# Optimization experiments

Measured on AMD Instinct MI355X. Metric: run time of the kernel, lower is better.

Reference implementation:

```python
import jax, jax.numpy as jnp
import numpy as np

INPUT, HIDDEN, OUTPUT = 128, 256, 128
BATCH, SEQ = 64, 2048


def setup_inputs() -> dict:
    key = jax.random.key(0)
    ks = jax.random.split(key, 7)
    s_ih = 1.0 / np.sqrt(HIDDEN)
    x = jax.random.normal(ks[0], (BATCH, SEQ, INPUT), dtype=jnp.float32)
    W_ih = jax.random.uniform(ks[1], (HIDDEN, INPUT), jnp.float32, -s_ih, s_ih)
    W_hh = jax.random.uniform(ks[2], (HIDDEN, HIDDEN), jnp.float32, -s_ih, s_ih)
    b_ih = jax.random.uniform(ks[3], (HIDDEN,), jnp.float32, -s_ih, s_ih)
    b_hh = jax.random.uniform(ks[4], (HIDDEN,), jnp.float32, -s_ih, s_ih)
    s_fc = 1.0 / np.sqrt(HIDDEN)
    W_fc = jax.random.uniform(ks[5], (OUTPUT, HIDDEN), jnp.float32, -s_fc, s_fc)
    b_fc = jax.random.uniform(ks[6], (OUTPUT,), jnp.float32, -s_fc, s_fc)
    return {"x": x, "W_ih": W_ih, "W_hh": W_hh, "b_ih": b_ih,
            "b_hh": b_hh, "W_fc": W_fc, "b_fc": b_fc}


def reference(x, W_ih, W_hh, b_ih, b_hh, W_fc, b_fc):
    B = x.shape[0]
    # Precompute input projections for all timesteps: [S, B, H]
    xp = jnp.einsum('bsi,hi->sbh', x, W_ih) + b_ih + b_hh
    h0 = jnp.zeros((B, W_hh.shape[0]), dtype=x.dtype)

    def step(h, xp_t):
        h = jnp.tanh(xp_t + h @ W_hh.T)
        return h, None

    hT, _ = jax.lax.scan(step, h0, xp)
    return hT @ W_fc.T + b_fc
```

## Files before the change

### kernel.cpp

```cpp
#include <hip/hip_runtime.h>
#include <hip/hip_bf16.h>
#include <hip/hip_fp16.h>


#define S_LEN 2048
#define B_SZ  64
#define IN_D  128
#define HID   256
#define OUT_D 128

typedef _Float16 half2_t __attribute__((ext_vector_type(2)));
typedef _Float16 half8_t __attribute__((ext_vector_type(8)));
typedef float    f32x4   __attribute__((ext_vector_type(4)));

#if __has_builtin(__builtin_amdgcn_fdot2)
#define FDOT2(a, b, c) __builtin_amdgcn_fdot2((a), (b), (c), false)
#else
#define FDOT2(a, b, c) ((c) + (float)(a).x * (float)(b).x + (float)(a).y * (float)(b).y)
#endif

#if __has_builtin(__builtin_amdgcn_exp2f)
#define EXP2F(x) __builtin_amdgcn_exp2f(x)
#else
#define EXP2F(x) exp2f(x)
#endif

__global__ __launch_bounds__(256) void xproj_kernel(
    const float* __restrict__ x, const float* __restrict__ W_ih,
    const float* __restrict__ b_ih, const float* __restrict__ b_hh,
    _Float16* __restrict__ xp)
{
    const int lane  = threadIdx.x & 63;
    const int wave  = threadIdx.x >> 6;
    const int r0    = blockIdx.x * 64 + wave * 16;
    const int idx16 = lane & 15;
    const int kq    = lane >> 4;

    half8_t afr[4];
    #pragma unroll
    for (int sl = 0; sl < 4; ++sl) {
        const float4* ap = (const float4*)(x + (size_t)(r0 + idx16) * IN_D + sl * 32 + kq * 8);
        float4 a0 = ap[0], a1 = ap[1];
        afr[sl] = half8_t{(_Float16)a0.x, (_Float16)a0.y, (_Float16)a0.z, (_Float16)a0.w,
                          (_Float16)a1.x, (_Float16)a1.y, (_Float16)a1.z, (_Float16)a1.w};
    }

    #pragma unroll 2
    for (int nc = 0; nc < 16; ++nc) {
        const int n0 = nc * 16;
        f32x4 acc = {0.f, 0.f, 0.f, 0.f};
        #pragma unroll
        for (int sl = 0; sl < 4; ++sl) {
            const float4* bp = (const float4*)(W_ih + (size_t)(n0 + idx16) * IN_D + sl * 32 + kq * 8);
            float4 b0 = bp[0], b1 = bp[1];
            half8_t bf = {(_Float16)b0.x, (_Float16)b0.y, (_Float16)b0.z, (_Float16)b0.w,
                          (_Float16)b1.x, (_Float16)b1.y, (_Float16)b1.z, (_Float16)b1.w};
            acc = __builtin_amdgcn_mfma_f32_16x16x32_f16(afr[sl], bf, acc, 0, 0, 0);
        }
        const float bias = b_ih[n0 + idx16] + b_hh[n0 + idx16];
        #pragma unroll
        for (int r = 0; r < 4; ++r) {
            const int m = r0 + kq * 4 + r;
            xp[(size_t)m * HID + n0 + idx16] = (_Float16)(acc[r] + bias);
        }
    }
}

__global__ __launch_bounds__(256, 1) void rnn_kernel(
    const _Float16* __restrict__ xp, const float* __restrict__ W_hh,
    const float* __restrict__ W_fc, const float* __restrict__ b_fc,
    float* __restrict__ out)
{
    const int b = blockIdx.x;
    const int j = threadIdx.x;

    __shared__ __align__(16) _Float16 hbuf[2][HID];

    half2_t w[128];
    {
        const float4* wr = (const float4*)(W_hh + (size_t)j * HID);
        #pragma unroll
        for (int c = 0; c < 64; ++c) {
            float4 v = wr[c];
            w[2 * c]     = half2_t{(_Float16)v.x, (_Float16)v.y};
            w[2 * c + 1] = half2_t{(_Float16)v.z, (_Float16)v.w};
        }
    }
    #pragma unroll
    for (int c = 0; c < 128; ++c) {
        asm volatile("" : "+v"(w[c]));
    }

    hbuf[0][j] = (_Float16)0.f;

    const _Float16* xpb = xp + (size_t)b * S_LEN * HID + j;
    _Float16 p0 = xpb[0];
    _Float16 p1 = xpb[HID];

    __syncthreads();

    for (int t = 0; t < S_LEN; ++t) {
        const int rb = t & 1;
        float a0 = 0.f, a1 = 0.f, a2 = 0.f, a3 = 0.f;
        const float4* hp = (const float4*)hbuf[rb];
        #pragma unroll
        for (int c = 0; c < 32; ++c) {
            float4 hv = hp[c];
            union { float f; half2_t h; } u0, u1, u2, u3;
            u0.f = hv.x; u1.f = hv.y; u2.f = hv.z; u3.f = hv.w;
            a0 = FDOT2(w[4 * c + 0], u0.h, a0);
            a1 = FDOT2(w[4 * c + 1], u1.h, a1);
            a2 = FDOT2(w[4 * c + 2], u2.h, a2);
            a3 = FDOT2(w[4 * c + 3], u3.h, a3);
        }
        const float acc = (a0 + a1) + (a2 + a3);

        const float xv = (float)p0;
        p0 = p1;
        const int tn = (t + 2 < S_LEN) ? (t + 2) : (S_LEN - 1);
        p1 = xpb[(size_t)tn * HID];

        const float z = acc + xv;
        const float e = EXP2F(z * 2.8853900817779268f);
        const float th = 1.f - 2.f / (e + 1.f);

        hbuf[rb ^ 1][j] = (_Float16)th;
        __syncthreads();
    }

    if (j < OUT_D) {
        float acc2 = b_fc[j];
        const float4* wp = (const float4*)(W_fc + (size_t)j * HID);
        const _Float16* hf = hbuf[0];
        #pragma unroll 8
        for (int c = 0; c < 64; ++c) {
            float4 wv = wp[c];
            acc2 += wv.x * (float)hf[4 * c + 0] + wv.y * (float)hf[4 * c + 1] +
                    wv.z * (float)hf[4 * c + 2] + wv.w * (float)hf[4 * c + 3];
        }
        out[(size_t)b * OUT_D + j] = acc2;
    }
}

extern "C" void kernel_launch(void* const* d_in, const int* in_sizes, int n_in,
                              void* d_out, int out_size, void* d_ws, size_t ws_size,
                              hipStream_t stream) {
    const float* x    = (const float*)d_in[0];
    const float* W_ih = (const float*)d_in[1];
    const float* W_hh = (const float*)d_in[2];
    const float* b_ih = (const float*)d_in[3];
    const float* b_hh = (const float*)d_in[4];
    const float* W_fc = (const float*)d_in[5];
    const float* b_fc = (const float*)d_in[6];
    float* outp = (float*)d_out;

    _Float16* xp_ws = (_Float16*)d_ws;

    dim3 gA(S_LEN * B_SZ / 64, 1, 1);
    xproj_kernel<<<gA, 256, 0, stream>>>(x, W_ih, b_ih, b_hh, xp_ws);

    rnn_kernel<<<B_SZ, HID, 0, stream>>>(xp_ws, W_hh, W_fc, b_fc, outp);
}
```

Before: 1.377 ms.

## Split recurrent dot product across four thread slices and enlarge xproj tiles

The recurrent kernel now uses 1024 threads per batch row, each covering a quarter of the hidden dimension, with the partial sums reduced through shared memory. This shortens the serial FDOT2 chain per step and reduces register pressure, at the cost of a second barrier each timestep. The projection kernel reuses each W_ih fragment across four M tiles, and the tanh division is replaced with a hardware reciprocal.

```diff
diff --git a/kernel.cpp b/kernel.cpp
--- a/kernel.cpp
+++ b/kernel.cpp
@@ -25,6 +25,12 @@
 #define EXP2F(x) exp2f(x)
 #endif
 
+#if __has_builtin(__builtin_amdgcn_rcpf)
+#define RCPF(x) __builtin_amdgcn_rcpf(x)
+#else
+#define RCPF(x) (1.0f / (x))
+#endif
+
 __global__ __launch_bounds__(256) void xproj_kernel(
     const float* __restrict__ x, const float* __restrict__ W_ih,
     const float* __restrict__ b_ih, const float* __restrict__ b_hh,
@@ -32,79 +38,89 @@
 {
     const int lane  = threadIdx.x & 63;
     const int wave  = threadIdx.x >> 6;
-    const int r0    = blockIdx.x * 64 + wave * 16;
     const int idx16 = lane & 15;
     const int kq    = lane >> 4;
+    const int r0    = blockIdx.x * 256 + wave * 64;
 
-    half8_t afr[4];
+    half8_t afr[4][4];
     #pragma unroll
-    for (int sl = 0; sl < 4; ++sl) {
-        const float4* ap = (const float4*)(x + (size_t)(r0 + idx16) * IN_D + sl * 32 + kq * 8);
-        float4 a0 = ap[0], a1 = ap[1];
-        afr[sl] = half8_t{(_Float16)a0.x, (_Float16)a0.y, (_Float16)a0.z, (_Float16)a0.w,
-                          (_Float16)a1.x, (_Float16)a1.y, (_Float16)a1.z, (_Float16)a1.w};
+    for (int mt = 0; mt < 4; ++mt) {
+        #pragma unroll
+        for (int sl = 0; sl < 4; ++sl) {
+            const float4* ap = (const float4*)(x + (size_t)(r0 + mt * 16 + idx16) * IN_D + sl * 32 + kq * 8);
+            float4 a0 = ap[0], a1 = ap[1];
+            afr[mt][sl] = half8_t{(_Float16)a0.x, (_Float16)a0.y, (_Float16)a0.z, (_Float16)a0.w,
+                                  (_Float16)a1.x, (_Float16)a1.y, (_Float16)a1.z, (_Float16)a1.w};
+        }
     }
 
-    #pragma unroll 2
     for (int nc = 0; nc < 16; ++nc) {
         const int n0 = nc * 16;
-        f32x4 acc = {0.f, 0.f, 0.f, 0.f};
+        const float bias = b_ih[n0 + idx16] + b_hh[n0 + idx16];
+
+        half8_t bfr[4];
         #pragma unroll
         for (int sl = 0; sl < 4; ++sl) {
             const float4* bp = (const float4*)(W_ih + (size_t)(n0 + idx16) * IN_D + sl * 32 + kq * 8);
             float4 b0 = bp[0], b1 = bp[1];
-            half8_t bf = {(_Float16)b0.x, (_Float16)b0.y, (_Float16)b0.z, (_Float16)b0.w,
-                          (_Float16)b1.x, (_Float16)b1.y, (_Float16)b1.z, (_Float16)b1.w};
-            acc = __builtin_amdgcn_mfma_f32_16x16x32_f16(afr[sl], bf, acc, 0, 0, 0);
+            bfr[sl] = half8_t{(_Float16)b0.x, (_Float16)b0.y, (_Float16)b0.z, (_Float16)b0.w,
+                              (_Float16)b1.x, (_Float16)b1.y, (_Float16)b1.z, (_Float16)b1.w};
         }
-        const float bias = b_ih[n0 + idx16] + b_hh[n0 + idx16];
+
         #pragma unroll
-        for (int r = 0; r < 4; ++r) {
-            const int m = r0 + kq * 4 + r;
-            xp[(size_t)m * HID + n0 + idx16] = (_Float16)(acc[r] + bias);
+        for (int mt = 0; mt < 4; ++mt) {
+            f32x4 acc = {0.f, 0.f, 0.f, 0.f};
+            #pragma unroll
+            for (int sl = 0; sl < 4; ++sl)
+                acc = __builtin_amdgcn_mfma_f32_16x16x32_f16(afr[mt][sl], bfr[sl], acc, 0, 0, 0);
+            #pragma unroll
+            for (int r = 0; r < 4; ++r) {
+                const int m = r0 + mt * 16 + kq * 4 + r;
+                xp[(size_t)m * HID + n0 + idx16] = (_Float16)(acc[r] + bias);
+            }
         }
     }
 }
 
-__global__ __launch_bounds__(256, 1) void rnn_kernel(
+__global__ __launch_bounds__(1024) void rnn_kernel(
     const _Float16* __restrict__ xp, const float* __restrict__ W_hh,
     const float* __restrict__ W_fc, const float* __restrict__ b_fc,
     float* __restrict__ out)
 {
-    const int b = blockIdx.x;
-    const int j = threadIdx.x;
+    const int b     = blockIdx.x;
+    const int tid   = threadIdx.x;
+    const int j     = tid & 255;
+    const int slice = tid >> 8;
 
     __shared__ __align__(16) _Float16 hbuf[2][HID];
+    __shared__ __align__(16) float    part[4][HID];
 
-    half2_t w[128];
+    half2_t w[32];
     {
-        const float4* wr = (const float4*)(W_hh + (size_t)j * HID);
+        const float4* wr = (const float4*)(W_hh + (size_t)j * HID + slice * 64);
         #pragma unroll
-        for (int c = 0; c < 64; ++c) {
+        for (int c = 0; c < 16; ++c) {
             float4 v = wr[c];
             w[2 * c]     = half2_t{(_Float16)v.x, (_Float16)v.y};
             w[2 * c + 1] = half2_t{(_Float16)v.z, (_Float16)v.w};
         }
     }
-    #pragma unroll
-    for (int c = 0; c < 128; ++c) {
-        asm volatile("" : "+v"(w[c]));
-    }
 
-    hbuf[0][j] = (_Float16)0.f;
+    if (tid < HID) hbuf[0][tid] = (_Float16)0.f;
 
+    const bool fin = (slice == (j >> 6));
     const _Float16* xpb = xp + (size_t)b * S_LEN * HID + j;
-    _Float16 p0 = xpb[0];
-    _Float16 p1 = xpb[HID];
+    float p0 = 0.f, p1 = 0.f;
+    if (fin) { p0 = (float)xpb[0]; p1 = (float)xpb[HID]; }
 
     __syncthreads();
 
     for (int t = 0; t < S_LEN; ++t) {
         const int rb = t & 1;
+        const float4* hp = (const float4*)&hbuf[rb][slice * 64];
         float a0 = 0.f, a1 = 0.f, a2 = 0.f, a3 = 0.f;
-        const float4* hp = (const float4*)hbuf[rb];
         #pragma unroll
-        for (int c = 0; c < 32; ++c) {
+        for (int c = 0; c < 8; ++c) {
             float4 hv = hp[c];
             union { float f; half2_t h; } u0, u1, u2, u3;
             u0.f = hv.x; u1.f = hv.y; u2.f = hv.z; u3.f = hv.w;
@@ -113,24 +129,23 @@
             a2 = FDOT2(w[4 * c + 2], u2.h, a2);
             a3 = FDOT2(w[4 * c + 3], u3.h, a3);
         }
-        const float acc = (a0 + a1) + (a2 + a3);
+        part[slice][j] = (a0 + a1) + (a2 + a3);
+        __syncthreads();
 
-        const float xv = (float)p0;
-        p0 = p1;
-        const int tn = (t + 2 < S_LEN) ? (t + 2) : (S_LEN - 1);
-        p1 = xpb[(size_t)tn * HID];
-
-        const float z = acc + xv;
-        const float e = EXP2F(z * 2.8853900817779268f);
-        const float th = 1.f - 2.f / (e + 1.f);
-
-        hbuf[rb ^ 1][j] = (_Float16)th;
+        if (fin) {
+            float z = part[0][j] + part[1][j] + part[2][j] + part[3][j] + p0;
+            p0 = p1;
+            const int tn = (t + 2 < S_LEN) ? (t + 2) : (S_LEN - 1);
+            p1 = (float)xpb[(size_t)tn * HID];
+            const float e = EXP2F(z * 2.8853900817779268f);
+            hbuf[rb ^ 1][j] = (_Float16)(1.f - 2.f * RCPF(e + 1.f));
+        }
         __syncthreads();
     }
 
-    if (j < OUT_D) {
-        float acc2 = b_fc[j];
-        const float4* wp = (const float4*)(W_fc + (size_t)j * HID);
+    if (tid < OUT_D) {
+        float acc2 = b_fc[tid];
+        const float4* wp = (const float4*)(W_fc + (size_t)tid * HID);
         const _Float16* hf = hbuf[0];
         #pragma unroll 8
         for (int c = 0; c < 64; ++c) {
@@ -138,7 +153,7 @@
             acc2 += wv.x * (float)hf[4 * c + 0] + wv.y * (float)hf[4 * c + 1] +
                     wv.z * (float)hf[4 * c + 2] + wv.w * (float)hf[4 * c + 3];
         }
-        out[(size_t)b * OUT_D + j] = acc2;
+        out[(size_t)b * OUT_D + tid] = acc2;
     }
 }
 
@@ -156,8 +171,8 @@
 
     _Float16* xp_ws = (_Float16*)d_ws;
 
-    dim3 gA(S_LEN * B_SZ / 64, 1, 1);
+    dim3 gA(S_LEN * B_SZ / 256, 1, 1);
     xproj_kernel<<<gA, 256, 0, stream>>>(x, W_ih, b_ih, b_hh, xp_ws);
 
-    rnn_kernel<<<B_SZ, HID, 0, stream>>>(xp_ws, W_hh, W_fc, b_fc, outp);
+    rnn_kernel<<<B_SZ, 1024, 0, stream>>>(xp_ws, W_hh, W_fc, b_fc, outp);
 }
```

New measurement: 1.553 ms. 12.8% more time.
